# Optimization experiments

Hardware: AMD Instinct MI355X
Metric: run time of the kernel (lower is better)

## Reference

```python
import jax, jax.numpy as jnp
import numpy as np
from jax import lax


def _combine(proj):
    # proj: [B,2,4,4]; returns 4x4 with top 3 rows = K[:3,:3] @ E[:3,:4]
    E = proj[:, 0]
    Km = proj[:, 1, :3, :3]
    top = jnp.einsum('bij,bjk->bik', Km, E[:, :3, :4])
    return jnp.concatenate([top, E[:, 3:4, :]], axis=1)


def _bilinear_sample(img, ix, iy):
    # img [B,C,H,W]; ix,iy [B,P] pixel coords (align_corners=True), zero padding
    B, C, H, W = img.shape
    x0 = jnp.floor(ix); y0 = jnp.floor(iy)
    x1 = x0 + 1.0; y1 = y0 + 1.0
    wx1 = ix - x0; wx0 = 1.0 - wx1
    wy1 = iy - y0; wy0 = 1.0 - wy1
    flat = img.reshape(B, C, H * W)
    def gather(xf, yf):
        valid = (xf >= 0) & (xf <= W - 1) & (yf >= 0) & (yf <= H - 1)
        xi = jnp.clip(xf, 0, W - 1).astype(jnp.int32)
        yi = jnp.clip(yf, 0, H - 1).astype(jnp.int32)
        idx = (yi * W + xi)[:, None, :]               # [B,1,P]
        v = jnp.take_along_axis(flat, idx, axis=2)    # [B,C,P]
        return v * valid[:, None, :].astype(img.dtype)
    return (gather(x0, y0) * (wx0 * wy0)[:, None, :]
          + gather(x1, y0) * (wx1 * wy0)[:, None, :]
          + gather(x0, y1) * (wx0 * wy1)[:, None, :]
          + gather(x1, y1) * (wx1 * wy1)[:, None, :])


def _homo_warp(src_fea, src_proj, ref_proj, depth_values):
    # MVSNet differentiable homography warping
    B, C, H, W = src_fea.shape
    D = depth_values.shape[1]
    proj = jnp.einsum('bij,bjk->bik', src_proj, jnp.linalg.inv(ref_proj))
    rot = proj[:, :3, :3]; trans = proj[:, :3, 3]
    yy, xx = jnp.meshgrid(jnp.arange(H, dtype=src_fea.dtype),
                          jnp.arange(W, dtype=src_fea.dtype), indexing='ij')
    xyz = jnp.stack([xx.ravel(), yy.ravel(), jnp.ones(H * W, src_fea.dtype)])  # [3,HW]
    rot_xyz = jnp.einsum('bij,jp->bip', rot, xyz)                              # [B,3,HW]
    pts = rot_xyz[:, :, None, :] * depth_values[:, None, :, None] \
        + trans[:, :, None, None]                                              # [B,3,D,HW]
    ix = (pts[:, 0] / pts[:, 2]).reshape(B, -1)
    iy = (pts[:, 1] / pts[:, 2]).reshape(B, -1)
    return _bilinear_sample(src_fea, ix, iy).reshape(B, C, D, H, W)


def _forward(features, proj_matrices, depth_values, w_reg, num_depth):
    B, V, C, H, W = features.shape
    D = num_depth
    ref_proj = _combine(proj_matrices[:, 0])
    ref_vol = jnp.broadcast_to(features[:, 0][:, :, None], (B, C, D, H, W))
    vol_sum = ref_vol
    vol_sq = ref_vol ** 2
    for v in range(1, V):  # fixed small number of views
        src_proj = _combine(proj_matrices[:, v])
        w = _homo_warp(features[:, v], src_proj, ref_proj, depth_values)
        vol_sum = vol_sum + w
        vol_sq = vol_sq + w ** 2
    variance = vol_sq / V - (vol_sum / V) ** 2
    # stand-in cost_regularization: single 3D conv C->1, k=3, SAME
    cost = lax.conv_general_dilated(variance, w_reg, (1, 1, 1), 'SAME',
                                    dimension_numbers=('NCDHW', 'OIDHW', 'NCDHW'))[:, 0]
    prob = jax.nn.softmax(cost, axis=1)
    # prev_state branch: is_begin is all-True (video start) -> warped_costvol == 0
    # (original then L1-normalizes prob_volume, overwriting itg_prob_volume)
    itg = prob / jnp.maximum(jnp.sum(jnp.abs(prob), axis=1, keepdims=True), 1e-12)
    depth = jnp.sum(itg * depth_values[:, :, None, None], axis=1)
    # photometric confidence (no_grad in original)
    padded = jnp.pad(prob, ((0, 0), (1, 2), (0, 0), (0, 0)))
    sum4 = lax.reduce_window(padded, 0.0, lax.add, (1, 4, 1, 1), (1, 1, 1, 1), 'VALID')
    di = jnp.sum(prob * jnp.arange(D, dtype=prob.dtype)[None, :, None, None], axis=1)
    di = jnp.clip(di.astype(jnp.int32), 0, D - 1)
    conf = jnp.take_along_axis(sum4, di[:, None], axis=1)[:, 0]
    return depth, conf, itg


def setup_inputs() -> dict:
    key = jax.random.key(0)
    k1, k2 = jax.random.split(key)
    B, V, C, D, H, W = 2, 5, 32, 48, 128, 160
    features = jax.random.normal(k1, (B, V, C, H, W), jnp.float32)
    f = 200.0
    K = np.eye(4, dtype=np.float32)
    K[0, 0] = f; K[1, 1] = f; K[0, 2] = W / 2.0; K[1, 2] = H / 2.0
    projs = []
    for v in range(V):
        E = np.eye(4, dtype=np.float32)
        E[0, 3] = 0.1 * v  # small camera baseline per view
        projs.append(np.stack([E, K]))
    proj_matrices = jnp.asarray(np.tile(np.stack(projs)[None], (B, 1, 1, 1, 1)))
    depth_values = jnp.tile(jnp.linspace(425.0, 935.0, D, dtype=jnp.float32)[None], (B, 1))
    w_reg = jax.random.normal(k2, (1, C, 3, 3, 3), jnp.float32) * 0.05
    is_begin = jnp.ones((B,), bool)
    return dict(features=features, proj_matrices=proj_matrices,
                depth_values=depth_values, w_reg=w_reg, is_begin=is_begin,
                num_depth=D, stage_idx=0)


def reference(features, proj_matrices, depth_values, w_reg, is_begin, num_depth, stage_idx):
    return _forward(features, proj_matrices, depth_values, w_reg, num_depth)
```

## Files before the change

kernel.cpp:

```cpp
#include <hip/hip_runtime.h>
#include <math.h>

constexpr int B_ = 2;
constexpr int V_ = 5;
constexpr int C_ = 32;
constexpr int D_ = 48;
constexpr int H_ = 128;
constexpr int W_ = 160;
constexpr int HW_ = H_ * W_;
constexpr int NVOX = B_ * D_ * HW_;
constexpr int PLANE = D_ * HW_;

typedef _Float16 half2_t __attribute__((ext_vector_type(2)));
typedef _Float16 half8_t __attribute__((ext_vector_type(8)));
typedef float floatx4 __attribute__((ext_vector_type(4)));


__device__ inline void combine4(const float* pm, float out[4][4]) {
    const float* E = pm;
    const float* K = pm + 16;
    for (int i = 0; i < 3; ++i)
        for (int j = 0; j < 4; ++j) {
            float a = 0.f;
            for (int k = 0; k < 3; ++k) a += K[i * 4 + k] * E[k * 4 + j];
            out[i][j] = a;
        }
    for (int j = 0; j < 4; ++j) out[3][j] = E[12 + j];
}

__device__ inline void invert4(const float A[4][4], float inv[4][4]) {
    float M[4][8];
    for (int i = 0; i < 4; ++i)
        for (int j = 0; j < 4; ++j) {
            M[i][j] = A[i][j];
            M[i][4 + j] = (i == j) ? 1.f : 0.f;
        }
    for (int col = 0; col < 4; ++col) {
        int piv = col;
        float best = fabsf(M[col][col]);
        for (int r = col + 1; r < 4; ++r) {
            float v = fabsf(M[r][col]);
            if (v > best) { best = v; piv = r; }
        }
        if (piv != col)
            for (int j = 0; j < 8; ++j) { float t = M[col][j]; M[col][j] = M[piv][j]; M[piv][j] = t; }
        float ip = 1.f / M[col][col];
        for (int j = 0; j < 8; ++j) M[col][j] *= ip;
        for (int r = 0; r < 4; ++r) {
            if (r == col) continue;
            float f = M[r][col];
            for (int j = 0; j < 8; ++j) M[r][j] -= f * M[col][j];
        }
    }
    for (int i = 0; i < 4; ++i)
        for (int j = 0; j < 4; ++j) inv[i][j] = M[i][4 + j];
}

__device__ inline unsigned bf_rne(float f) {
    unsigned u = __float_as_uint(f);
    return (u + 0x7FFFu + ((u >> 16) & 1u)) >> 16;
}

__device__ inline float bflo(unsigned u) { return __uint_as_float(u << 16); }
__device__ inline float bfhi(unsigned u) { return __uint_as_float(u & 0xffff0000u); }

__device__ inline unsigned h2pack(float a, float b) {
    unsigned lo = (unsigned)__builtin_bit_cast(unsigned short, (_Float16)a);
    unsigned hi = (unsigned)__builtin_bit_cast(unsigned short, (_Float16)b);
    return lo | (hi << 16);
}

__device__ inline unsigned cvt_pk_bf16(float a, float b) {
    unsigned r;
    asm("v_cvt_pk_bf16_f32 %0, %1, %2" : "=v"(r) : "v"(a), "v"(b));
    return r;
}

__global__ void setup_kernel(const float* __restrict__ proj, const float* __restrict__ wreg,
                             float* __restrict__ rt, unsigned* __restrict__ wtb) {
    int t = threadIdx.x;
    if (t < B_) {
        int b = t;
        float ref[4][4], inv[4][4];
        combine4(proj + (size_t)((b * V_ + 0) * 2) * 16, ref);
        invert4(ref, inv);
        for (int v = 1; v < V_; ++v) {
            float src[4][4];
            combine4(proj + (size_t)((b * V_ + v) * 2) * 16, src);
            float P[3][4];
            for (int i = 0; i < 3; ++i)
                for (int j = 0; j < 4; ++j) {
                    float a = 0.f;
                    for (int k = 0; k < 4; ++k) a += src[i][k] * inv[k][j];
                    P[i][j] = a;
                }
            float* o = rt + (size_t)(b * (V_ - 1) + (v - 1)) * 12;
            o[0] = P[0][0]; o[1] = P[0][1]; o[2] = P[0][2];
            o[3] = P[1][0]; o[4] = P[1][1]; o[5] = P[1][2];
            o[6] = P[2][0]; o[7] = P[2][1]; o[8] = P[2][2];
            o[9] = P[0][3]; o[10] = P[1][3]; o[11] = P[2][3];
        }
    }
    if (t < 128) {
        int i = t >> 6;
        int lane = t & 63;
        int q = lane >> 4;
        int l = lane & 15;
        int tap = i * 16 + l;
        unsigned u[4];
#pragma unroll
        for (int jj = 0; jj < 4; ++jj) {
            int ch0 = q * 8 + 2 * jj;
            float v0 = (tap < 27) ? wreg[ch0 * 27 + tap] : 0.f;
            float v1 = (tap < 27) ? wreg[(ch0 + 1) * 27 + tap] : 0.f;
            u[jj] = h2pack(v0, v1);
        }
        uint4* o = (uint4*)wtb;
        o[i * 64 + lane] = make_uint4(u[0], u[1], u[2], u[3]);
    }
}

__global__ __launch_bounds__(256) void transpose_kernel(const float* __restrict__ feat,
                                                        unsigned* __restrict__ feat_cl) {
    int idx = blockIdx.x * 256 + threadIdx.x;
    if (idx >= B_ * V_ * HW_) return;
    int pix = idx % HW_;
    int bv = idx / HW_;
    const float* src = feat + (size_t)bv * C_ * HW_ + pix;
    unsigned u[16];
#pragma unroll
    for (int j = 0; j < 16; ++j)
        u[j] = h2pack(src[(size_t)(2 * j) * HW_], src[(size_t)(2 * j + 1) * HW_]);
    uint4* dst = (uint4*)(feat_cl + (size_t)idx * 16);
    dst[0] = make_uint4(u[0], u[1], u[2], u[3]);
    dst[1] = make_uint4(u[4], u[5], u[6], u[7]);
    dst[2] = make_uint4(u[8], u[9], u[10], u[11]);
    dst[3] = make_uint4(u[12], u[13], u[14], u[15]);
}

__global__ __launch_bounds__(256) void warp_kernel(const unsigned char* __restrict__ fb,
                                                   const float* __restrict__ rt,
                                                   const float* __restrict__ dv,
                                                   const unsigned* __restrict__ wtb,
                                                   unsigned short* __restrict__ T) {
    const int tid = threadIdx.x;
    const int lane = tid & 63;
    const int cq = tid & 3;
    const unsigned cq16 = (unsigned)cq << 4;
    const int b = blockIdx.z;
    const int d = blockIdx.y;
    const int pixb = blockIdx.x * 64;
    const int pix = pixb + (tid >> 2);
    const int w = pix % W_;
    const int h = pix / W_;
    const float wf = (float)w, hf = (float)h;
    const float dep = dv[b * D_ + d];

    const uint4* wp = (const uint4*)wtb;
    uint4 a0u = wp[lane];
    uint4 a1u = wp[64 + lane];

    unsigned W00u, W01u, W10u, W11u;
    int pix00, pix01, pix10, pix11;
    {
        const float* m = rt + (b * (V_ - 1) + cq) * 12;
        float xp = fmaf(fmaf(m[0], wf, fmaf(m[1], hf, m[2])), dep, m[9]);
        float yp = fmaf(fmaf(m[3], wf, fmaf(m[4], hf, m[5])), dep, m[10]);
        float zp = fmaf(fmaf(m[6], wf, fmaf(m[7], hf, m[8])), dep, m[11]);
        float iz = __builtin_amdgcn_rcpf(zp);
        float ix = xp * iz, iy = yp * iz;
        float x0f = floorf(ix), y0f = floorf(iy);
        float wx1 = ix - x0f, wx0 = 1.f - wx1;
        float wy1 = iy - y0f, wy0 = 1.f - wy1;
        float x1f = x0f + 1.f, y1f = y0f + 1.f;
        float wx0v = (x0f >= 0.f && x0f <= (float)(W_ - 1)) ? wx0 : 0.f;
        float wx1v = (x1f >= 0.f && x1f <= (float)(W_ - 1)) ? wx1 : 0.f;
        float wy0v = (y0f >= 0.f && y0f <= (float)(H_ - 1)) ? wy0 : 0.f;
        float wy1v = (y1f >= 0.f && y1f <= (float)(H_ - 1)) ? wy1 : 0.f;
        int x0i = (int)fminf(fmaxf(x0f, 0.f), (float)(W_ - 1));
        int x1i = (int)fminf(fmaxf(x1f, 0.f), (float)(W_ - 1));
        int y0i = (int)fminf(fmaxf(y0f, 0.f), (float)(H_ - 1));
        int y1i = (int)fminf(fmaxf(y1f, 0.f), (float)(H_ - 1));
        float w00 = wx0v * wy0v, w01 = wx1v * wy0v;
        float w10 = wx0v * wy1v, w11 = wx1v * wy1v;
        W00u = __builtin_bit_cast(unsigned, __builtin_amdgcn_cvt_pkrtz(w00, w00));
        W01u = __builtin_bit_cast(unsigned, __builtin_amdgcn_cvt_pkrtz(w01, w01));
        W10u = __builtin_bit_cast(unsigned, __builtin_amdgcn_cvt_pkrtz(w10, w10));
        W11u = __builtin_bit_cast(unsigned, __builtin_amdgcn_cvt_pkrtz(w11, w11));
        pix00 = y0i * W_ + x0i;
        pix01 = y0i * W_ + x1i;
        pix10 = y1i * W_ + x0i;
        pix11 = y1i * W_ + x1i;
    }

    half2_t s2[4], q2[4];
    {
        const unsigned char* rb = fb + (size_t)(b * V_) * HW_ * 64;
        uint4 r = *(const uint4*)(rb + (((unsigned)pix) << 6) + cq16);
        unsigned ru[4] = {r.x, r.y, r.z, r.w};
#pragma unroll
        for (int jj = 0; jj < 4; ++jj) {
            half2_t f = __builtin_bit_cast(half2_t, ru[jj]);
            s2[jj] = f;
            q2[jj] = f * f;
        }
    }

#pragma unroll
    for (int v = 0; v < V_ - 1; ++v) {
        int sl = (lane & ~3) | v;
        half2_t Wa = __builtin_bit_cast(half2_t, (unsigned)__shfl((int)W00u, sl));
        half2_t Wb = __builtin_bit_cast(half2_t, (unsigned)__shfl((int)W01u, sl));
        half2_t Wc = __builtin_bit_cast(half2_t, (unsigned)__shfl((int)W10u, sl));
        half2_t Wd = __builtin_bit_cast(half2_t, (unsigned)__shfl((int)W11u, sl));
        unsigned O00 = ((unsigned)__shfl(pix00, sl) << 6) + cq16;
        unsigned O01 = ((unsigned)__shfl(pix01, sl) << 6) + cq16;
        unsigned O10 = ((unsigned)__shfl(pix10, sl) << 6) + cq16;
        unsigned O11 = ((unsigned)__shfl(pix11, sl) << 6) + cq16;
        const unsigned char* base = fb + (size_t)(b * V_ + v + 1) * HW_ * 64;
        uint4 c0 = *(const uint4*)(base + O00);
        uint4 c1 = *(const uint4*)(base + O01);
        uint4 c2 = *(const uint4*)(base + O10);
        uint4 c3 = *(const uint4*)(base + O11);
        unsigned u0[4] = {c0.x, c0.y, c0.z, c0.w};
        unsigned u1[4] = {c1.x, c1.y, c1.z, c1.w};
        unsigned u2[4] = {c2.x, c2.y, c2.z, c2.w};
        unsigned u3[4] = {c3.x, c3.y, c3.z, c3.w};
#pragma unroll
        for (int jj = 0; jj < 4; ++jj) {
            half2_t acc = __builtin_bit_cast(half2_t, u0[jj]) * Wa
                        + __builtin_bit_cast(half2_t, u1[jj]) * Wb
                        + __builtin_bit_cast(half2_t, u2[jj]) * Wc
                        + __builtin_bit_cast(half2_t, u3[jj]) * Wd;
            s2[jj] += acc;
            q2[jj] += acc * acc;
        }
    }

    const _Float16 ivh = (_Float16)(1.0f / (float)V_);
    const half2_t iv2 = {ivh, ivh};
    unsigned pk[4];
#pragma unroll
    for (int jj = 0; jj < 4; ++jj) {
        half2_t ms = s2[jj] * iv2;
        half2_t var = q2[jj] * iv2 - ms * ms;
        pk[jj] = __builtin_bit_cast(unsigned, var);
    }

    uint4 bu;
    {
        int srcl = ((lane & 15) << 2) + (lane >> 4);
        bu.x = (unsigned)__shfl((int)pk[0], srcl);
        bu.y = (unsigned)__shfl((int)pk[1], srcl);
        bu.z = (unsigned)__shfl((int)pk[2], srcl);
        bu.w = (unsigned)__shfl((int)pk[3], srcl);
    }
    half8_t bfrag = __builtin_bit_cast(half8_t, bu);
    half8_t afrag0 = __builtin_bit_cast(half8_t, a0u);
    half8_t afrag1 = __builtin_bit_cast(half8_t, a1u);

    floatx4 z = {0.f, 0.f, 0.f, 0.f};
    floatx4 t0 = __builtin_amdgcn_mfma_f32_16x16x32_f16(afrag0, bfrag, z, 0, 0, 0);
    floatx4 t1 = __builtin_amdgcn_mfma_f32_16x16x32_f16(afrag1, bfrag, z, 0, 0, 0);

    const unsigned gidx = (unsigned)(b * PLANE + d * HW_ + pixb + ((tid >> 6) << 4) + (lane & 15));
    const int tq = (lane >> 4) << 2;
    {
        unsigned u01 = cvt_pk_bf16(t0[0], t0[1]);
        unsigned u23 = cvt_pk_bf16(t0[2], t0[3]);
        T[(unsigned)((tq + 0) * NVOX) + gidx] = (unsigned short)(u01 & 0xffffu);
        T[(unsigned)((tq + 1) * NVOX) + gidx] = (unsigned short)(u01 >> 16);
        T[(unsigned)((tq + 2) * NVOX) + gidx] = (unsigned short)(u23 & 0xffffu);
        T[(unsigned)((tq + 3) * NVOX) + gidx] = (unsigned short)(u23 >> 16);
    }
    if (tq < 12) {
        unsigned u01 = cvt_pk_bf16(t1[0], t1[1]);
        T[(unsigned)((16 + tq) * NVOX) + gidx] = (unsigned short)(u01 & 0xffffu);
        T[(unsigned)((17 + tq) * NVOX) + gidx] = (unsigned short)(u01 >> 16);
        if (tq < 8) {
            unsigned u23 = cvt_pk_bf16(t1[2], t1[3]);
            T[(unsigned)((18 + tq) * NVOX) + gidx] = (unsigned short)(u23 & 0xffffu);
            T[(unsigned)((19 + tq) * NVOX) + gidx] = (unsigned short)(u23 >> 16);
        } else {
            T[(unsigned)(26 * NVOX) + gidx] = (unsigned short)bf_rne(t1[2]);
        }
    }
}

__global__ __launch_bounds__(256) void cost_kernel(const unsigned short* __restrict__ T,
                                                   float* __restrict__ cost) {
    int t = blockIdx.x * 256 + threadIdx.x;
    int v0 = t * 8;
    int w0 = v0 % W_;
    int h = (v0 / W_) % H_;
    int d = (v0 / HW_) % D_;
    int b = v0 / PLANE;
    float acc[8];
#pragma unroll
    for (int i = 0; i < 8; ++i) acc[i] = 0.f;

#pragma unroll
    for (int kd = 0; kd < 3; ++kd) {
        int dd = d + kd - 1;
        if (dd < 0 || dd >= D_) continue;
#pragma unroll
        for (int kh = 0; kh < 3; ++kh) {
            int hh = h + kh - 1;
            if (hh < 0 || hh >= H_) continue;
            unsigned r = (unsigned)(b * PLANE + dd * HW_ + hh * W_);
            int j = kd * 9 + kh * 3;
            const unsigned short* p0 = T + (size_t)j * NVOX + r;
            const unsigned short* p1 = p0 + NVOX;
            const unsigned short* p2 = p1 + NVOX;
            uint4 A0 = *(const uint4*)(p0 + w0);
            uint4 A1 = *(const uint4*)(p1 + w0);
            uint4 A2 = *(const uint4*)(p2 + w0);
            float eL = (w0 > 0) ? bflo((unsigned)p0[w0 - 1]) : 0.f;
            float eR = (w0 + 8 < W_) ? bflo((unsigned)p2[w0 + 8]) : 0.f;
            unsigned x0[4] = {A0.x, A0.y, A0.z, A0.w};
            unsigned x1[4] = {A1.x, A1.y, A1.z, A1.w};
            unsigned x2[4] = {A2.x, A2.y, A2.z, A2.w};
            float a0[8], a1[8], a2[8];
#pragma unroll
            for (int k = 0; k < 4; ++k) {
                a0[2 * k] = bflo(x0[k]); a0[2 * k + 1] = bfhi(x0[k]);
                a1[2 * k] = bflo(x1[k]); a1[2 * k + 1] = bfhi(x1[k]);
                a2[2 * k] = bflo(x2[k]); a2[2 * k + 1] = bfhi(x2[k]);
            }
            acc[0] += eL + a1[0] + a2[1];
#pragma unroll
            for (int i = 1; i < 7; ++i) acc[i] += a0[i - 1] + a1[i] + a2[i + 1];
            acc[7] += a0[6] + a1[7] + eR;
        }
    }
    float4* cp = (float4*)(cost + v0);
    cp[0] = make_float4(acc[0], acc[1], acc[2], acc[3]);
    cp[1] = make_float4(acc[4], acc[5], acc[6], acc[7]);
}

__global__ __launch_bounds__(256) void out_kernel(const float* __restrict__ cost,
                                                  const float* __restrict__ dv,
                                                  float* __restrict__ out) {
    __shared__ float red[4][64];
    const int tid = threadIdx.x;
    const int lane = tid & 63;
    const int wq = tid >> 6;
    const int pixg = blockIdx.x * 64 + lane;
    const int b = pixg / HW_;
    const int pix = pixg - b * HW_;
    const float* cb = cost + (size_t)b * PLANE + pix;

    float p[12];
    float mx = -1e30f;
#pragma unroll
    for (int i = 0; i < 12; ++i) {
        p[i] = cb[(size_t)(wq * 12 + i) * HW_];
        mx = fmaxf(mx, p[i]);
    }
    red[wq][lane] = mx;
    __syncthreads();
    mx = fmaxf(fmaxf(red[0][lane], red[1][lane]), fmaxf(red[2][lane], red[3][lane]));
    float S = 0.f;
#pragma unroll
    for (int i = 0; i < 12; ++i) {
        p[i] = expf(p[i] - mx);
        S += p[i];
    }
    __syncthreads();
    red[wq][lane] = S;
    __syncthreads();
    S = red[0][lane] + red[1][lane] + red[2][lane] + red[3][lane];
    float invS = 1.f / S;
    float S2p = 0.f;
#pragma unroll
    for (int i = 0; i < 12; ++i) {
        p[i] *= invS;
        S2p += p[i];
    }
    __syncthreads();
    red[wq][lane] = S2p;
    __syncthreads();
    float S2 = red[0][lane] + red[1][lane] + red[2][lane] + red[3][lane];
    float invS2 = 1.f / fmaxf(S2, 1e-12f);
    float dp = 0.f, difp = 0.f;
#pragma unroll
    for (int i = 0; i < 12; ++i) {
        int d0 = wq * 12 + i;
        dp = fmaf(p[i] * invS2, dv[b * D_ + d0], dp);
        difp = fmaf(p[i], (float)d0, difp);
    }
    __syncthreads();
    red[wq][lane] = dp;
    __syncthreads();
    float depth = red[0][lane] + red[1][lane] + red[2][lane] + red[3][lane];
    __syncthreads();
    red[wq][lane] = difp;
    __syncthreads();
    float dif = red[0][lane] + red[1][lane] + red[2][lane] + red[3][lane];
    int di = (int)dif;
    di = min(max(di, 0), D_ - 1);
    float cf = 0.f;
#pragma unroll
    for (int i = 0; i < 12; ++i) {
        int d0 = wq * 12 + i;
        if (d0 >= di - 1 && d0 <= di + 2) cf += p[i];
    }
    __syncthreads();
    red[wq][lane] = cf;
    __syncthreads();
    float conf = red[0][lane] + red[1][lane] + red[2][lane] + red[3][lane];

    if (wq == 0) {
        out[pixg] = depth;
        out[B_ * HW_ + pixg] = conf;
    }
    float* itg = out + 2 * B_ * HW_ + (size_t)b * PLANE + pix;
#pragma unroll
    for (int i = 0; i < 12; ++i)
        itg[(size_t)(wq * 12 + i) * HW_] = p[i] * invS2;
}

extern "C" void kernel_launch(void* const* d_in, const int* in_sizes, int n_in,
                              void* d_out, int out_size, void* d_ws, size_t ws_size,
                              hipStream_t stream) {
    const float* feat = (const float*)d_in[0];
    const float* proj = (const float*)d_in[1];
    const float* dv   = (const float*)d_in[2];
    const float* wreg = (const float*)d_in[3];
    float* out = (float*)d_out;
    float* ws = (float*)d_ws;

    const size_t rt_off = 0;
    const size_t rt_sz = 128;
    const size_t wtb_off = rt_off + rt_sz;
    const size_t wtb_sz = 512;
    const size_t fcl_off = wtb_off + wtb_sz;
    const size_t fcl_sz = (size_t)B_ * V_ * HW_ * 16;
    const size_t T_off = fcl_off + fcl_sz;
    const size_t T_sz = (size_t)27 * NVOX / 2;
    const size_t cost_off = T_off + T_sz;
    const size_t cost_sz = (size_t)NVOX;
    const size_t need = (cost_off + cost_sz) * sizeof(float);
    if (ws_size < need) return;

    float* rt = ws + rt_off;
    unsigned* wtb = (unsigned*)(ws + wtb_off);
    unsigned* feat_cl = (unsigned*)(ws + fcl_off);
    unsigned short* T = (unsigned short*)(ws + T_off);
    float* cost = ws + cost_off;

    setup_kernel<<<1, 128, 0, stream>>>(proj, wreg, rt, wtb);
    transpose_kernel<<<(B_ * V_ * HW_) / 256, 256, 0, stream>>>(feat, feat_cl);
    dim3 wgrid(HW_ / 64, D_, B_);
    warp_kernel<<<wgrid, 256, 0, stream>>>((const unsigned char*)feat_cl, rt, dv, wtb, T);
    cost_kernel<<<(NVOX / 8) / 256, 256, 0, stream>>>(T, cost);
    out_kernel<<<(B_ * HW_) / 64, 256, 0, stream>>>(cost, dv, out);
}
```

Before: 200.1 us.

## Assign one source view per lane and transpose results via xor-shuffle exchange

Each of the four lanes in a pixel group now gathers all 64 bytes of channels for its own source view, using its own bilinear weights and offsets. Previously each lane covered a channel quarter across all views, which needed eight shuffles per view to broadcast weights and pixel indices. The per-view results are then redistributed to the channel-quarter layout with a two-stage butterfly of shfl_xor exchanges before the variance accumulation. This removes the broadcast shuffles and makes each lane read contiguous 64-byte rows, at the cost of 16 live accumulator registers and 16 shuffles in the transpose.

```diff
diff --git a/kernel.cpp b/kernel.cpp
--- a/kernel.cpp
+++ b/kernel.cpp
@@ -145,8 +145,8 @@
                                                    unsigned short* __restrict__ T) {
     const int tid = threadIdx.x;
     const int lane = tid & 63;
-    const int cq = tid & 3;
-    const unsigned cq16 = (unsigned)cq << 4;
+    const int j = tid & 3;
+    const unsigned cq16 = (unsigned)j << 4;
     const int b = blockIdx.z;
     const int d = blockIdx.y;
     const int pixb = blockIdx.x * 64;
@@ -160,10 +160,23 @@
     uint4 a0u = wp[lane];
     uint4 a1u = wp[64 + lane];
 
+    half2_t s2[4], q2[4];
+    {
+        const unsigned char* rb = fb + (size_t)(b * V_) * HW_ * 64;
+        uint4 r = *(const uint4*)(rb + (((unsigned)pix) << 6) + cq16);
+        unsigned ru[4] = {r.x, r.y, r.z, r.w};
+#pragma unroll
+        for (int jj = 0; jj < 4; ++jj) {
+            half2_t f = __builtin_bit_cast(half2_t, ru[jj]);
+            s2[jj] = f;
+            q2[jj] = f * f;
+        }
+    }
+
     unsigned W00u, W01u, W10u, W11u;
-    int pix00, pix01, pix10, pix11;
+    unsigned O00, O01, O10, O11;
     {
-        const float* m = rt + (b * (V_ - 1) + cq) * 12;
+        const float* m = rt + (b * (V_ - 1) + j) * 12;
         float xp = fmaf(fmaf(m[0], wf, fmaf(m[1], hf, m[2])), dep, m[9]);
         float yp = fmaf(fmaf(m[3], wf, fmaf(m[4], hf, m[5])), dep, m[10]);
         float zp = fmaf(fmaf(m[6], wf, fmaf(m[7], hf, m[8])), dep, m[11]);
@@ -187,54 +200,72 @@
         W01u = __builtin_bit_cast(unsigned, __builtin_amdgcn_cvt_pkrtz(w01, w01));
         W10u = __builtin_bit_cast(unsigned, __builtin_amdgcn_cvt_pkrtz(w10, w10));
         W11u = __builtin_bit_cast(unsigned, __builtin_amdgcn_cvt_pkrtz(w11, w11));
-        pix00 = y0i * W_ + x0i;
-        pix01 = y0i * W_ + x1i;
-        pix10 = y1i * W_ + x0i;
-        pix11 = y1i * W_ + x1i;
-    }
-
-    half2_t s2[4], q2[4];
+        O00 = (unsigned)(y0i * W_ + x0i) << 6;
+        O01 = (unsigned)(y0i * W_ + x1i) << 6;
+        O10 = (unsigned)(y1i * W_ + x0i) << 6;
+        O11 = (unsigned)(y1i * W_ + x1i) << 6;
+    }
+
+    unsigned A[4][4];
     {
-        const unsigned char* rb = fb + (size_t)(b * V_) * HW_ * 64;
-        uint4 r = *(const uint4*)(rb + (((unsigned)pix) << 6) + cq16);
-        unsigned ru[4] = {r.x, r.y, r.z, r.w};
+        const unsigned char* base = fb + (size_t)(b * V_ + j + 1) * HW_ * 64;
+        half2_t Wa = __builtin_bit_cast(half2_t, W00u);
+        half2_t Wb = __builtin_bit_cast(half2_t, W01u);
+        half2_t Wc = __builtin_bit_cast(half2_t, W10u);
+        half2_t Wd = __builtin_bit_cast(half2_t, W11u);
+#pragma unroll
+        for (int q = 0; q < 4; ++q) {
+            uint4 c0 = *(const uint4*)(base + O00 + q * 16);
+            uint4 c1 = *(const uint4*)(base + O01 + q * 16);
+            uint4 c2 = *(const uint4*)(base + O10 + q * 16);
+            uint4 c3 = *(const uint4*)(base + O11 + q * 16);
+            unsigned u0[4] = {c0.x, c0.y, c0.z, c0.w};
+            unsigned u1[4] = {c1.x, c1.y, c1.z, c1.w};
+            unsigned u2[4] = {c2.x, c2.y, c2.z, c2.w};
+            unsigned u3[4] = {c3.x, c3.y, c3.z, c3.w};
+#pragma unroll
+            for (int jj = 0; jj < 4; ++jj) {
+                half2_t acc = __builtin_bit_cast(half2_t, u0[jj]) * Wa
+                            + __builtin_bit_cast(half2_t, u1[jj]) * Wb
+                            + __builtin_bit_cast(half2_t, u2[jj]) * Wc
+                            + __builtin_bit_cast(half2_t, u3[jj]) * Wd;
+                A[q][jj] = __builtin_bit_cast(unsigned, acc);
+            }
+        }
+    }
+
+    const bool b0 = (j & 1) != 0;
+    const bool b1 = (j & 2) != 0;
+    unsigned Ra[2][4], Rb[2][4];
+#pragma unroll
+    for (int k = 0; k < 2; ++k)
 #pragma unroll
         for (int jj = 0; jj < 4; ++jj) {
-            half2_t f = __builtin_bit_cast(half2_t, ru[jj]);
-            s2[jj] = f;
-            q2[jj] = f * f;
-        }
-    }
-
-#pragma unroll
-    for (int v = 0; v < V_ - 1; ++v) {
-        int sl = (lane & ~3) | v;
-        half2_t Wa = __builtin_bit_cast(half2_t, (unsigned)__shfl((int)W00u, sl));
-        half2_t Wb = __builtin_bit_cast(half2_t, (unsigned)__shfl((int)W01u, sl));
-        half2_t Wc = __builtin_bit_cast(half2_t, (unsigned)__shfl((int)W10u, sl));
-        half2_t Wd = __builtin_bit_cast(half2_t, (unsigned)__shfl((int)W11u, sl));
-        unsigned O00 = ((unsigned)__shfl(pix00, sl) << 6) + cq16;
-        unsigned O01 = ((unsigned)__shfl(pix01, sl) << 6) + cq16;
-        unsigned O10 = ((unsigned)__shfl(pix10, sl) << 6) + cq16;
-        unsigned O11 = ((unsigned)__shfl(pix11, sl) << 6) + cq16;
-        const unsigned char* base = fb + (size_t)(b * V_ + v + 1) * HW_ * 64;
-        uint4 c0 = *(const uint4*)(base + O00);
-        uint4 c1 = *(const uint4*)(base + O01);
-        uint4 c2 = *(const uint4*)(base + O10);
-        uint4 c3 = *(const uint4*)(base + O11);
-        unsigned u0[4] = {c0.x, c0.y, c0.z, c0.w};
-        unsigned u1[4] = {c1.x, c1.y, c1.z, c1.w};
-        unsigned u2[4] = {c2.x, c2.y, c2.z, c2.w};
-        unsigned u3[4] = {c3.x, c3.y, c3.z, c3.w};
-#pragma unroll
-        for (int jj = 0; jj < 4; ++jj) {
-            half2_t acc = __builtin_bit_cast(half2_t, u0[jj]) * Wa
-                        + __builtin_bit_cast(half2_t, u1[jj]) * Wb
-                        + __builtin_bit_cast(half2_t, u2[jj]) * Wc
-                        + __builtin_bit_cast(half2_t, u3[jj]) * Wd;
-            s2[jj] += acc;
-            q2[jj] += acc * acc;
-        }
+            unsigned snd = b0 ? A[2 * k][jj] : A[2 * k + 1][jj];
+            unsigned rcv = (unsigned)__shfl_xor((int)snd, 1);
+            Ra[k][jj] = b0 ? A[2 * k + 1][jj] : A[2 * k][jj];
+            Rb[k][jj] = rcv;
+        }
+    unsigned B0[4], B1[4], B2[4], B3[4];
+#pragma unroll
+    for (int jj = 0; jj < 4; ++jj) {
+        unsigned sndA = b1 ? Ra[0][jj] : Ra[1][jj];
+        unsigned sndB = b1 ? Rb[0][jj] : Rb[1][jj];
+        B0[jj] = b1 ? Ra[1][jj] : Ra[0][jj];
+        B1[jj] = b1 ? Rb[1][jj] : Rb[0][jj];
+        B2[jj] = (unsigned)__shfl_xor((int)sndA, 2);
+        B3[jj] = (unsigned)__shfl_xor((int)sndB, 2);
+    }
+
+#pragma unroll
+    for (int jj = 0; jj < 4; ++jj) {
+        half2_t v0 = __builtin_bit_cast(half2_t, B0[jj]);
+        half2_t v1 = __builtin_bit_cast(half2_t, B1[jj]);
+        half2_t v2 = __builtin_bit_cast(half2_t, B2[jj]);
+        half2_t v3 = __builtin_bit_cast(half2_t, B3[jj]);
+        s2[jj] += v0; s2[jj] += v1; s2[jj] += v2; s2[jj] += v3;
+        q2[jj] += v0 * v0; q2[jj] += v1 * v1;
+        q2[jj] += v2 * v2; q2[jj] += v3 * v3;
     }
 
     const _Float16 ivh = (_Float16)(1.0f / (float)V_);
```

Measured after the change: 351.2 us. 75.5% more time.
